# Kernel tuning notes

Measured on AMD Instinct MI355X. Metric: run time of the kernel, lower is better.

The kernel has to match this reference:

```python
import jax, jax.numpy as jnp
import numpy as np

N_NODES = 100000
N_EDGES = 1600000
IN_DIM = 256
HID = 128
ALPHA = 0.1
K_STEPS = 10


def setup_inputs() -> dict:
    key = jax.random.key(0)
    ks = jax.random.split(key, 10)
    x = jax.random.normal(ks[0], (N_NODES, IN_DIM), dtype=jnp.float32)
    edge_index = jax.random.randint(ks[1], (2, N_EDGES), 0, N_NODES, dtype=jnp.int64)
    s = 0.02
    W1 = jax.random.normal(ks[2], (HID, IN_DIM), dtype=jnp.float32) * s
    b1 = jnp.zeros((HID,), dtype=jnp.float32)
    W2 = jax.random.normal(ks[3], (HID, HID), dtype=jnp.float32) * s
    b2 = jnp.zeros((HID,), dtype=jnp.float32)
    W3 = jax.random.normal(ks[4], (HID, HID), dtype=jnp.float32) * s
    b3 = jnp.zeros((HID,), dtype=jnp.float32)
    Wo = jax.random.normal(ks[5], (1, HID), dtype=jnp.float32) * s
    bo = jnp.zeros((1,), dtype=jnp.float32)
    return {"x": x, "edge_index": edge_index, "W1": W1, "b1": b1,
            "W2": W2, "b2": b2, "W3": W3, "b3": b3, "Wo": Wo, "bo": bo}


def _gcn_norm(edge_index, num_nodes):
    # add self-loops, then symmetric normalization 1/sqrt(deg_i * deg_j)
    loop = jnp.arange(num_nodes, dtype=edge_index.dtype)
    src = jnp.concatenate([edge_index[0], loop])
    dst = jnp.concatenate([edge_index[1], loop])
    ones = jnp.ones(src.shape[0], dtype=jnp.float32)
    deg = jax.ops.segment_sum(ones, dst, num_segments=num_nodes)
    dinv = jnp.where(deg > 0, jax.lax.rsqrt(deg), 0.0)
    norm = dinv[src] * dinv[dst]
    return src, dst, norm


def reference(x, edge_index, W1, b1, W2, b2, W3, b3, Wo, bo):
    # MLP encoder (dropout=0 -> identity in eval)
    h = jax.nn.relu(x @ W1.T + b1)
    h = jax.nn.relu(h @ W2.T + b2)
    h = jax.nn.relu(h @ W3.T + b3)
    # APPNP propagation: h <- (1-alpha) * A_hat h + alpha * h0
    n = x.shape[0]
    src, dst, norm = _gcn_norm(edge_index, n)
    h0 = h
    for _ in range(K_STEPS):
        msg = norm[:, None] * h[src]            # [E+N, HID]
        agg = jax.ops.segment_sum(msg, dst, num_segments=n)
        h = (1.0 - ALPHA) * agg + ALPHA * h0
    out = h @ Wo.T + bo                          # [N, 1]
    return out.squeeze(-1)
```

## Files before the change

### kernel.cpp

```cpp
#include <hip/hip_runtime.h>

#define NN   100000
#define NE   1600000
#define IND  256
#define HIDD 128
#define BCAP 64
#define NPART 196
#define SCAP 10240
#define HPITCH 136

typedef __attribute__((ext_vector_type(8))) short short8v;
typedef __attribute__((ext_vector_type(4))) float f32x4;

__device__ inline unsigned packbf2(float x, float y) {
  unsigned xb = __float_as_uint(x);
  unsigned yb = __float_as_uint(y);
  xb += 0x7fffu + ((xb >> 16) & 1u);
  yb += 0x7fffu + ((yb >> 16) & 1u);
  return (xb >> 16) | (yb & 0xffff0000u);
}
__device__ inline unsigned short bf16r(float x) {
  unsigned b = __float_as_uint(x);
  b += 0x7fffu + ((b >> 16) & 1u);
  return (unsigned short)(b >> 16);
}

__global__ void wcvt_all(const float* __restrict__ W1, const float* __restrict__ W2,
                         const float* __restrict__ W3, unsigned* __restrict__ W1b,
                         unsigned* __restrict__ W2b, unsigned* __restrict__ W3b) {
  int i = blockIdx.x * 256 + threadIdx.x;
  const float* src; unsigned* dst; int off;
  if (i < 16384)      { src = W1; dst = W1b; off = i; }
  else if (i < 24576) { src = W2; dst = W2b; off = i - 16384; }
  else                { src = W3; dst = W3b; off = i - 24576; }
  float2 v = ((const float2*)src)[off];
  dst[off] = packbf2(v.x, v.y);
}

__global__ __launch_bounds__(256, 8) void fill_phaseA(
    const int* __restrict__ src, const int* __restrict__ dst,
    int* __restrict__ gcur, unsigned* __restrict__ sbuf)
{
  __shared__ int hist[NPART];
  __shared__ int lofs[NPART];
  const int tid = threadIdx.x;
  const int base = blockIdx.x * 2048;
  for (int i = tid; i < NPART; i += 256) hist[i] = 0;
  __syncthreads();
  int d[8], s[8];
#pragma unroll
  for (int i = 0; i < 8; ++i) {
    int e = base + i * 256 + tid;
    bool v = e < NE;
    d[i] = v ? dst[e] : -1;
    s[i] = v ? src[e] : 0;
    if (v) atomicAdd(&hist[d[i] >> 9], 1);
  }
  __syncthreads();
  for (int i = tid; i < NPART; i += 256)
    lofs[i] = atomicAdd(&gcur[i], hist[i]);
  __syncthreads();
#pragma unroll
  for (int i = 0; i < 8; ++i) {
    if (d[i] >= 0) {
      int p = d[i] >> 9;
      int q = atomicAdd(&lofs[p], 1);
      if (q < SCAP)
        sbuf[(size_t)p * SCAP + q] = ((unsigned)(d[i] & 511) << 17) | (unsigned)s[i];
    }
  }
}

__global__ __launch_bounds__(256, 8) void fill_phaseB(
    const unsigned* __restrict__ sbuf, const int* __restrict__ gcur,
    int* __restrict__ colbuk, int* __restrict__ deg)
{
  __shared__ int lcur[512];
  const int tid = threadIdx.x;
  const int b = blockIdx.x;
  for (int i = tid; i < 512; i += 256) lcur[i] = 0;
  __syncthreads();
  int cnt = min(gcur[b], SCAP);
  const unsigned* sp = sbuf + (size_t)b * SCAP;
  for (int i = tid; i < cnt; i += 256) {
    unsigned u = sp[i];
    int dloc = (int)(u >> 17);
    int s = (int)(u & 0x1FFFFu);
    int pos = atomicAdd(&lcur[dloc], 1);
    if (pos < BCAP) colbuk[(size_t)((b << 9) + dloc) * BCAP + pos] = s;
  }
  __syncthreads();
  for (int i = tid; i < 512; i += 256) {
    int node = (b << 9) + i;
    if (node < NN) deg[node] = lcur[i];
  }
}

__global__ __launch_bounds__(256) void enc_fused(
    const float* __restrict__ x,
    const unsigned short* __restrict__ W1b, const float* __restrict__ b1,
    const unsigned short* __restrict__ W2b, const float* __restrict__ b2,
    const unsigned short* __restrict__ W3b, const float* __restrict__ b3,
    const float* __restrict__ Wo, float* __restrict__ z)
{
  __shared__ unsigned short hbuf[128 * HPITCH];
  __shared__ float zsh[2][128];
  const int tid = threadIdx.x;
  const int lane = tid & 63, wid = tid >> 6;
  const int wr = wid >> 1, wc = wid & 1;
  const int bm = blockIdx.x * 128;
  const int lr = lane & 15, lg = lane >> 4;

  f32x4 acc[4][4];
#pragma unroll
  for (int i = 0; i < 4; ++i)
#pragma unroll
    for (int j = 0; j < 4; ++j) acc[i][j] = (f32x4){0.f, 0.f, 0.f, 0.f};

  for (int k0 = 0; k0 < IND; k0 += 32) {
    short8v a[4], b[4];
#pragma unroll
    for (int i = 0; i < 4; ++i) {
      int grow = bm + wr * 64 + i * 16 + lr;
      uint4 pk = make_uint4(0u, 0u, 0u, 0u);
      if (grow < NN) {
        const float* ap = x + (size_t)grow * IND + k0 + lg * 8;
        float4 v0 = ((const float4*)ap)[0];
        float4 v1 = ((const float4*)ap)[1];
        pk.x = packbf2(v0.x, v0.y); pk.y = packbf2(v0.z, v0.w);
        pk.z = packbf2(v1.x, v1.y); pk.w = packbf2(v1.z, v1.w);
      }
      a[i] = *(short8v*)&pk;
    }
#pragma unroll
    for (int j = 0; j < 4; ++j)
      b[j] = *(const short8v*)&W1b[(size_t)(wc * 64 + j * 16 + lr) * IND + k0 + lg * 8];
#pragma unroll
    for (int i = 0; i < 4; ++i)
#pragma unroll
      for (int j = 0; j < 4; ++j)
        acc[i][j] = __builtin_amdgcn_mfma_f32_16x16x32_bf16(a[i], b[j], acc[i][j], 0, 0, 0);
  }
#pragma unroll
  for (int i = 0; i < 4; ++i)
#pragma unroll
    for (int e = 0; e < 4; ++e) {
      int lrow = wr * 64 + i * 16 + lg * 4 + e;
#pragma unroll
      for (int j = 0; j < 4; ++j) {
        int cc = wc * 64 + j * 16 + lr;
        hbuf[lrow * HPITCH + cc] = bf16r(fmaxf(acc[i][j][e] + b1[cc], 0.f));
      }
    }
  __syncthreads();

#pragma unroll
  for (int i = 0; i < 4; ++i)
#pragma unroll
    for (int j = 0; j < 4; ++j) acc[i][j] = (f32x4){0.f, 0.f, 0.f, 0.f};
  for (int k0 = 0; k0 < HIDD; k0 += 32) {
    short8v a[4], b[4];
#pragma unroll
    for (int i = 0; i < 4; ++i)
      a[i] = *(const short8v*)&hbuf[(wr * 64 + i * 16 + lr) * HPITCH + k0 + lg * 8];
#pragma unroll
    for (int j = 0; j < 4; ++j)
      b[j] = *(const short8v*)&W2b[(size_t)(wc * 64 + j * 16 + lr) * HIDD + k0 + lg * 8];
#pragma unroll
    for (int i = 0; i < 4; ++i)
#pragma unroll
      for (int j = 0; j < 4; ++j)
        acc[i][j] = __builtin_amdgcn_mfma_f32_16x16x32_bf16(a[i], b[j], acc[i][j], 0, 0, 0);
  }
  __syncthreads();
#pragma unroll
  for (int i = 0; i < 4; ++i)
#pragma unroll
    for (int e = 0; e < 4; ++e) {
      int lrow = wr * 64 + i * 16 + lg * 4 + e;
#pragma unroll
      for (int j = 0; j < 4; ++j) {
        int cc = wc * 64 + j * 16 + lr;
        hbuf[lrow * HPITCH + cc] = bf16r(fmaxf(acc[i][j][e] + b2[cc], 0.f));
      }
    }
  __syncthreads();

#pragma unroll
  for (int i = 0; i < 4; ++i)
#pragma unroll
    for (int j = 0; j < 4; ++j) acc[i][j] = (f32x4){0.f, 0.f, 0.f, 0.f};
  for (int k0 = 0; k0 < HIDD; k0 += 32) {
    short8v a[4], b[4];
#pragma unroll
    for (int i = 0; i < 4; ++i)
      a[i] = *(const short8v*)&hbuf[(wr * 64 + i * 16 + lr) * HPITCH + k0 + lg * 8];
#pragma unroll
    for (int j = 0; j < 4; ++j)
      b[j] = *(const short8v*)&W3b[(size_t)(wc * 64 + j * 16 + lr) * HIDD + k0 + lg * 8];
#pragma unroll
    for (int i = 0; i < 4; ++i)
#pragma unroll
      for (int j = 0; j < 4; ++j)
        acc[i][j] = __builtin_amdgcn_mfma_f32_16x16x32_bf16(a[i], b[j], acc[i][j], 0, 0, 0);
  }
  float wv[4];
#pragma unroll
  for (int j = 0; j < 4; ++j) wv[j] = Wo[wc * 64 + j * 16 + lr];
  zsh[tid >> 7][tid & 127] = 0.f;
  __syncthreads();
#pragma unroll
  for (int i = 0; i < 4; ++i)
#pragma unroll
    for (int e = 0; e < 4; ++e) {
      float part = 0.f;
#pragma unroll
      for (int j = 0; j < 4; ++j) {
        int cc = wc * 64 + j * 16 + lr;
        part += fmaxf(acc[i][j][e] + b3[cc], 0.f) * wv[j];
      }
#pragma unroll
      for (int off = 8; off > 0; off >>= 1) part += __shfl_down(part, off, 16);
      if (lr == 0) zsh[wc][wr * 64 + i * 16 + lg * 4 + e] = part;
    }
  __syncthreads();
  if (tid < 128) {
    int row = bm + tid;
    if (row < NN) z[row] = zsh[0][tid] + zsh[1][tid];
  }
}

__global__ void prep_scalar(const int* __restrict__ deg, const float* __restrict__ z,
                            float* __restrict__ dinv, float* __restrict__ va) {
  int i = blockIdx.x * 256 + threadIdx.x;
  if (i < NN) {
    float di = rsqrtf((float)(deg[i] + 1));
    dinv[i] = di;
    va[i] = di * z[i];
  }
}

template<int LAST>
__global__ __launch_bounds__(256, 8) void appnp_sstep(
    const float* __restrict__ vin, const float* __restrict__ z,
    const float* __restrict__ dinv, const int* __restrict__ deg,
    const int* __restrict__ colbuk, float* __restrict__ vout,
    const float* __restrict__ bo, float* __restrict__ out)
{
  int tid = threadIdx.x;
  int sl = tid & 15;
  int node = blockIdx.x * 16 + (tid >> 4);
  if (node >= NN) return;
  int m = min(deg[node], BCAP);
  float val = (sl == 0) ? vin[node] : 0.f;
  for (int j = sl; j < m; j += 16)
    val += vin[colbuk[(size_t)node * BCAP + j]];
#pragma unroll
  for (int off = 8; off > 0; off >>= 1) val += __shfl_down(val, off, 16);
  if (sl == 0) {
    float di = dinv[node];
    float s = 0.9f * di * val + 0.1f * z[node];
    if (LAST) out[node] = s + bo[0];
    else vout[node] = di * s;
  }
}

extern "C" void kernel_launch(void* const* d_in, const int* in_sizes, int n_in,
                              void* d_out, int out_size, void* d_ws, size_t ws_size,
                              hipStream_t stream) {
  const float* x   = (const float*)d_in[0];
  const int*   ei  = (const int*)d_in[1];
  const float* W1  = (const float*)d_in[2];
  const float* b1  = (const float*)d_in[3];
  const float* W2  = (const float*)d_in[4];
  const float* b2  = (const float*)d_in[5];
  const float* W3  = (const float*)d_in[6];
  const float* b3  = (const float*)d_in[7];
  const float* Wo  = (const float*)d_in[8];
  const float* bo  = (const float*)d_in[9];
  float* out = (float*)d_out;

  const int* srcv = ei;
  const int* dstv = ei + NE;

  int*      colbuk = (int*)d_ws;
  unsigned* sbuf   = (unsigned*)(colbuk + (size_t)NN * BCAP);
  int*      gcur   = (int*)(sbuf + (size_t)NPART * SCAP);
  int*      deg    = gcur + NPART;
  float*    dinv   = (float*)(deg + NN);
  float*    zbuf   = dinv + NN;
  float*    va     = zbuf + NN;
  float*    vb     = va + NN;
  unsigned* W1b    = (unsigned*)(vb + NN);
  unsigned* W2b    = W1b + 16384;
  unsigned* W3b    = W2b + 8192;

  hipMemsetAsync(gcur, 0, NPART * 4, stream);

  wcvt_all<<<128, 256, 0, stream>>>(W1, W2, W3, W1b, W2b, W3b);

  fill_phaseA<<<(NE + 2047) / 2048, 256, 0, stream>>>(srcv, dstv, gcur, sbuf);
  fill_phaseB<<<NPART, 256, 0, stream>>>(sbuf, gcur, colbuk, deg);

  const int ng = (NN + 127) / 128;
  enc_fused<<<ng, 256, 0, stream>>>(x, (unsigned short*)W1b, b1,
                                    (unsigned short*)W2b, b2,
                                    (unsigned short*)W3b, b3, Wo, zbuf);

  prep_scalar<<<(NN + 255) / 256, 256, 0, stream>>>(deg, zbuf, dinv, va);

  int ssb = (NN + 15) / 16;
  float* cur = va; float* nxt = vb;
  for (int k = 0; k < 9; ++k) {
    appnp_sstep<0><<<ssb, 256, 0, stream>>>(cur, zbuf, dinv, deg, colbuk,
                                            nxt, nullptr, nullptr);
    float* t = cur; cur = nxt; nxt = t;
  }
  appnp_sstep<1><<<ssb, 256, 0, stream>>>(cur, zbuf, dinv, deg, colbuk,
                                          nullptr, bo, out);
}
```

Before: 235.9 us.

## Finer edge partitions, fuse degree/scalar prep, stage encoder input via LDS

Edge bucketing now uses 782 partitions of 128 nodes instead of 196 of 512, which gives fill_phaseB more blocks and smaller LDS counters. dinv is computed in fill_phaseB and the va scaling in enc_fused, so the prep_scalar kernel launch goes away. The first encoder GEMM stages the bf16-converted x tile through LDS with coalesced row loads instead of per-lane strided global reads. This adds two barriers per k-step, and SCAP=2500 per partition relies on there being few overflows given the random degree distribution.

```diff
diff --git a/kernel.cpp b/kernel.cpp
--- a/kernel.cpp
+++ b/kernel.cpp
@@ -5,8 +5,9 @@
 #define IND  256
 #define HIDD 128
 #define BCAP 64
-#define NPART 196
-#define SCAP 10240
+#define NPART 782
+#define SCAP 2500
+#define APITCH 40
 #define HPITCH 136
 
 typedef __attribute__((ext_vector_type(8))) short short8v;
@@ -54,31 +55,31 @@
     bool v = e < NE;
     d[i] = v ? dst[e] : -1;
     s[i] = v ? src[e] : 0;
-    if (v) atomicAdd(&hist[d[i] >> 9], 1);
+    if (v) atomicAdd(&hist[d[i] >> 7], 1);
   }
   __syncthreads();
   for (int i = tid; i < NPART; i += 256)
-    lofs[i] = atomicAdd(&gcur[i], hist[i]);
+    lofs[i] = hist[i] ? atomicAdd(&gcur[i], hist[i]) : 0;
   __syncthreads();
 #pragma unroll
   for (int i = 0; i < 8; ++i) {
     if (d[i] >= 0) {
-      int p = d[i] >> 9;
+      int p = d[i] >> 7;
       int q = atomicAdd(&lofs[p], 1);
       if (q < SCAP)
-        sbuf[(size_t)p * SCAP + q] = ((unsigned)(d[i] & 511) << 17) | (unsigned)s[i];
+        sbuf[(size_t)p * SCAP + q] = ((unsigned)(d[i] & 127) << 17) | (unsigned)s[i];
     }
   }
 }
 
 __global__ __launch_bounds__(256, 8) void fill_phaseB(
     const unsigned* __restrict__ sbuf, const int* __restrict__ gcur,
-    int* __restrict__ colbuk, int* __restrict__ deg)
+    int* __restrict__ colbuk, int* __restrict__ deg, float* __restrict__ dinv)
 {
-  __shared__ int lcur[512];
+  __shared__ int lcur[128];
   const int tid = threadIdx.x;
   const int b = blockIdx.x;
-  for (int i = tid; i < 512; i += 256) lcur[i] = 0;
+  if (tid < 128) lcur[tid] = 0;
   __syncthreads();
   int cnt = min(gcur[b], SCAP);
   const unsigned* sp = sbuf + (size_t)b * SCAP;
@@ -87,12 +88,16 @@
     int dloc = (int)(u >> 17);
     int s = (int)(u & 0x1FFFFu);
     int pos = atomicAdd(&lcur[dloc], 1);
-    if (pos < BCAP) colbuk[(size_t)((b << 9) + dloc) * BCAP + pos] = s;
-  }
-  __syncthreads();
-  for (int i = tid; i < 512; i += 256) {
-    int node = (b << 9) + i;
-    if (node < NN) deg[node] = lcur[i];
+    if (pos < BCAP) colbuk[(size_t)((b << 7) + dloc) * BCAP + pos] = s;
+  }
+  __syncthreads();
+  if (tid < 128) {
+    int node = (b << 7) + tid;
+    if (node < NN) {
+      int dg = lcur[tid];
+      deg[node] = dg;
+      dinv[node] = rsqrtf((float)(dg + 1));
+    }
   }
 }
 
@@ -101,10 +106,12 @@
     const unsigned short* __restrict__ W1b, const float* __restrict__ b1,
     const unsigned short* __restrict__ W2b, const float* __restrict__ b2,
     const unsigned short* __restrict__ W3b, const float* __restrict__ b3,
-    const float* __restrict__ Wo, float* __restrict__ z)
+    const float* __restrict__ Wo, const float* __restrict__ dinv,
+    float* __restrict__ z, float* __restrict__ va)
 {
   __shared__ unsigned short hbuf[128 * HPITCH];
   __shared__ float zsh[2][128];
+  unsigned short* lA = hbuf;
   const int tid = threadIdx.x;
   const int lane = tid & 63, wid = tid >> 6;
   const int wr = wid >> 1, wc = wid & 1;
@@ -118,28 +125,36 @@
     for (int j = 0; j < 4; ++j) acc[i][j] = (f32x4){0.f, 0.f, 0.f, 0.f};
 
   for (int k0 = 0; k0 < IND; k0 += 32) {
-    short8v a[4], b[4];
-#pragma unroll
-    for (int i = 0; i < 4; ++i) {
-      int grow = bm + wr * 64 + i * 16 + lr;
-      uint4 pk = make_uint4(0u, 0u, 0u, 0u);
+#pragma unroll
+    for (int s0 = 0; s0 < 512; s0 += 256) {
+      int s = s0 + tid, rr = s >> 2, g = s & 3;
+      int grow = bm + rr;
+      float4 v0 = make_float4(0.f, 0.f, 0.f, 0.f), v1 = v0;
       if (grow < NN) {
-        const float* ap = x + (size_t)grow * IND + k0 + lg * 8;
-        float4 v0 = ((const float4*)ap)[0];
-        float4 v1 = ((const float4*)ap)[1];
-        pk.x = packbf2(v0.x, v0.y); pk.y = packbf2(v0.z, v0.w);
-        pk.z = packbf2(v1.x, v1.y); pk.w = packbf2(v1.z, v1.w);
+        const float* ap = x + (size_t)grow * IND + k0 + g * 8;
+        v0 = ((const float4*)ap)[0]; v1 = ((const float4*)ap)[1];
       }
-      a[i] = *(short8v*)&pk;
-    }
-#pragma unroll
-    for (int j = 0; j < 4; ++j)
-      b[j] = *(const short8v*)&W1b[(size_t)(wc * 64 + j * 16 + lr) * IND + k0 + lg * 8];
-#pragma unroll
-    for (int i = 0; i < 4; ++i)
+      uint4 pk;
+      pk.x = packbf2(v0.x, v0.y); pk.y = packbf2(v0.z, v0.w);
+      pk.z = packbf2(v1.x, v1.y); pk.w = packbf2(v1.z, v1.w);
+      *(uint4*)&lA[rr * APITCH + g * 8] = pk;
+    }
+    __syncthreads();
+    {
+      short8v a[4], b[4];
+#pragma unroll
+      for (int i = 0; i < 4; ++i)
+        a[i] = *(const short8v*)&lA[(wr * 64 + i * 16 + lr) * APITCH + lg * 8];
 #pragma unroll
       for (int j = 0; j < 4; ++j)
-        acc[i][j] = __builtin_amdgcn_mfma_f32_16x16x32_bf16(a[i], b[j], acc[i][j], 0, 0, 0);
+        b[j] = *(const short8v*)&W1b[(size_t)(wc * 64 + j * 16 + lr) * IND + k0 + lg * 8];
+#pragma unroll
+      for (int i = 0; i < 4; ++i)
+#pragma unroll
+        for (int j = 0; j < 4; ++j)
+          acc[i][j] = __builtin_amdgcn_mfma_f32_16x16x32_bf16(a[i], b[j], acc[i][j], 0, 0, 0);
+    }
+    __syncthreads();
   }
 #pragma unroll
   for (int i = 0; i < 4; ++i)
@@ -226,17 +241,11 @@
   __syncthreads();
   if (tid < 128) {
     int row = bm + tid;
-    if (row < NN) z[row] = zsh[0][tid] + zsh[1][tid];
-  }
-}
-
-__global__ void prep_scalar(const int* __restrict__ deg, const float* __restrict__ z,
-                            float* __restrict__ dinv, float* __restrict__ va) {
-  int i = blockIdx.x * 256 + threadIdx.x;
-  if (i < NN) {
-    float di = rsqrtf((float)(deg[i] + 1));
-    dinv[i] = di;
-    va[i] = di * z[i];
+    if (row < NN) {
+      float zv = zsh[0][tid] + zsh[1][tid];
+      z[row] = zv;
+      va[row] = dinv[row] * zv;
+    }
   }
 }
 
@@ -300,14 +309,13 @@
   wcvt_all<<<128, 256, 0, stream>>>(W1, W2, W3, W1b, W2b, W3b);
 
   fill_phaseA<<<(NE + 2047) / 2048, 256, 0, stream>>>(srcv, dstv, gcur, sbuf);
-  fill_phaseB<<<NPART, 256, 0, stream>>>(sbuf, gcur, colbuk, deg);
+  fill_phaseB<<<NPART, 256, 0, stream>>>(sbuf, gcur, colbuk, deg, dinv);
 
   const int ng = (NN + 127) / 128;
   enc_fused<<<ng, 256, 0, stream>>>(x, (unsigned short*)W1b, b1,
                                     (unsigned short*)W2b, b2,
-                                    (unsigned short*)W3b, b3, Wo, zbuf);
-
-  prep_scalar<<<(NN + 255) / 256, 256, 0, stream>>>(deg, zbuf, dinv, va);
+                                    (unsigned short*)W3b, b3, Wo, dinv,
+                                    zbuf, va);
 
   int ssb = (NN + 15) / 16;
   float* cur = va; float* nxt = vb;
```

New measurement: 238.4 us. No clear change (+1.0%).

## Restructure encoder to per-wave 16-row tiles and fold scalar prep into fill

Applied to the files above, without the earlier changes.

The fused MLP encoder now gives each wave its own 16-row tile covering all 128 output columns, with private LDS scratch and no block-level barriers, instead of a 128-row block tile shared by four waves. The prep_scalar kernel is removed: its degree, dinv and initial-vector work moves into fill_phaseB, which now runs after the encoder so z is available. fill_phaseA also skips global atomics for empty histogram bins. The intent is to remove barrier stalls and one kernel launch. In exchange, each wave reloads the full weight matrices from global/L2 with less reuse per load, and the encoder row loop assumes NN is a multiple of 16.

```diff
diff --git a/kernel.cpp b/kernel.cpp
--- a/kernel.cpp
+++ b/kernel.cpp
@@ -7,7 +7,7 @@
 #define BCAP 64
 #define NPART 196
 #define SCAP 10240
-#define HPITCH 136
+#define HP   136
 
 typedef __attribute__((ext_vector_type(8))) short short8v;
 typedef __attribute__((ext_vector_type(4))) float f32x4;
@@ -58,7 +58,7 @@
   }
   __syncthreads();
   for (int i = tid; i < NPART; i += 256)
-    lofs[i] = atomicAdd(&gcur[i], hist[i]);
+    lofs[i] = hist[i] ? atomicAdd(&gcur[i], hist[i]) : 0;
   __syncthreads();
 #pragma unroll
   for (int i = 0; i < 8; ++i) {
@@ -73,7 +73,8 @@
 
 __global__ __launch_bounds__(256, 8) void fill_phaseB(
     const unsigned* __restrict__ sbuf, const int* __restrict__ gcur,
-    int* __restrict__ colbuk, int* __restrict__ deg)
+    const float* __restrict__ z, int* __restrict__ colbuk,
+    int* __restrict__ deg, float* __restrict__ dinv, float* __restrict__ va)
 {
   __shared__ int lcur[512];
   const int tid = threadIdx.x;
@@ -92,7 +93,13 @@
   __syncthreads();
   for (int i = tid; i < 512; i += 256) {
     int node = (b << 9) + i;
-    if (node < NN) deg[node] = lcur[i];
+    if (node < NN) {
+      int dg = lcur[i];
+      float di = rsqrtf((float)(dg + 1));
+      deg[node] = dg;
+      dinv[node] = di;
+      va[node] = di * z[node];
+    }
   }
 }
 
@@ -103,140 +110,91 @@
     const unsigned short* __restrict__ W3b, const float* __restrict__ b3,
     const float* __restrict__ Wo, float* __restrict__ z)
 {
-  __shared__ unsigned short hbuf[128 * HPITCH];
-  __shared__ float zsh[2][128];
+  __shared__ unsigned short hl[4][16 * HP];
   const int tid = threadIdx.x;
   const int lane = tid & 63, wid = tid >> 6;
-  const int wr = wid >> 1, wc = wid & 1;
-  const int bm = blockIdx.x * 128;
   const int lr = lane & 15, lg = lane >> 4;
-
-  f32x4 acc[4][4];
-#pragma unroll
-  for (int i = 0; i < 4; ++i)
-#pragma unroll
-    for (int j = 0; j < 4; ++j) acc[i][j] = (f32x4){0.f, 0.f, 0.f, 0.f};
-
-  for (int k0 = 0; k0 < IND; k0 += 32) {
-    short8v a[4], b[4];
-#pragma unroll
-    for (int i = 0; i < 4; ++i) {
-      int grow = bm + wr * 64 + i * 16 + lr;
-      uint4 pk = make_uint4(0u, 0u, 0u, 0u);
-      if (grow < NN) {
-        const float* ap = x + (size_t)grow * IND + k0 + lg * 8;
-        float4 v0 = ((const float4*)ap)[0];
-        float4 v1 = ((const float4*)ap)[1];
-        pk.x = packbf2(v0.x, v0.y); pk.y = packbf2(v0.z, v0.w);
-        pk.z = packbf2(v1.x, v1.y); pk.w = packbf2(v1.z, v1.w);
-      }
-      a[i] = *(short8v*)&pk;
-    }
-#pragma unroll
-    for (int j = 0; j < 4; ++j)
-      b[j] = *(const short8v*)&W1b[(size_t)(wc * 64 + j * 16 + lr) * IND + k0 + lg * 8];
-#pragma unroll
-    for (int i = 0; i < 4; ++i)
-#pragma unroll
-      for (int j = 0; j < 4; ++j)
-        acc[i][j] = __builtin_amdgcn_mfma_f32_16x16x32_bf16(a[i], b[j], acc[i][j], 0, 0, 0);
-  }
-#pragma unroll
-  for (int i = 0; i < 4; ++i)
-#pragma unroll
-    for (int e = 0; e < 4; ++e) {
-      int lrow = wr * 64 + i * 16 + lg * 4 + e;
-#pragma unroll
-      for (int j = 0; j < 4; ++j) {
-        int cc = wc * 64 + j * 16 + lr;
-        hbuf[lrow * HPITCH + cc] = bf16r(fmaxf(acc[i][j][e] + b1[cc], 0.f));
-      }
-    }
-  __syncthreads();
-
-#pragma unroll
-  for (int i = 0; i < 4; ++i)
-#pragma unroll
-    for (int j = 0; j < 4; ++j) acc[i][j] = (f32x4){0.f, 0.f, 0.f, 0.f};
-  for (int k0 = 0; k0 < HIDD; k0 += 32) {
-    short8v a[4], b[4];
-#pragma unroll
-    for (int i = 0; i < 4; ++i)
-      a[i] = *(const short8v*)&hbuf[(wr * 64 + i * 16 + lr) * HPITCH + k0 + lg * 8];
-#pragma unroll
-    for (int j = 0; j < 4; ++j)
-      b[j] = *(const short8v*)&W2b[(size_t)(wc * 64 + j * 16 + lr) * HIDD + k0 + lg * 8];
-#pragma unroll
-    for (int i = 0; i < 4; ++i)
-#pragma unroll
-      for (int j = 0; j < 4; ++j)
-        acc[i][j] = __builtin_amdgcn_mfma_f32_16x16x32_bf16(a[i], b[j], acc[i][j], 0, 0, 0);
-  }
-  __syncthreads();
-#pragma unroll
-  for (int i = 0; i < 4; ++i)
-#pragma unroll
-    for (int e = 0; e < 4; ++e) {
-      int lrow = wr * 64 + i * 16 + lg * 4 + e;
-#pragma unroll
-      for (int j = 0; j < 4; ++j) {
-        int cc = wc * 64 + j * 16 + lr;
-        hbuf[lrow * HPITCH + cc] = bf16r(fmaxf(acc[i][j][e] + b2[cc], 0.f));
-      }
-    }
-  __syncthreads();
-
-#pragma unroll
-  for (int i = 0; i < 4; ++i)
-#pragma unroll
-    for (int j = 0; j < 4; ++j) acc[i][j] = (f32x4){0.f, 0.f, 0.f, 0.f};
-  for (int k0 = 0; k0 < HIDD; k0 += 32) {
-    short8v a[4], b[4];
-#pragma unroll
-    for (int i = 0; i < 4; ++i)
-      a[i] = *(const short8v*)&hbuf[(wr * 64 + i * 16 + lr) * HPITCH + k0 + lg * 8];
-#pragma unroll
-    for (int j = 0; j < 4; ++j)
-      b[j] = *(const short8v*)&W3b[(size_t)(wc * 64 + j * 16 + lr) * HIDD + k0 + lg * 8];
-#pragma unroll
-    for (int i = 0; i < 4; ++i)
-#pragma unroll
-      for (int j = 0; j < 4; ++j)
-        acc[i][j] = __builtin_amdgcn_mfma_f32_16x16x32_bf16(a[i], b[j], acc[i][j], 0, 0, 0);
-  }
-  float wv[4];
-#pragma unroll
-  for (int j = 0; j < 4; ++j) wv[j] = Wo[wc * 64 + j * 16 + lr];
-  zsh[tid >> 7][tid & 127] = 0.f;
-  __syncthreads();
-#pragma unroll
-  for (int i = 0; i < 4; ++i)
-#pragma unroll
-    for (int e = 0; e < 4; ++e) {
-      float part = 0.f;
-#pragma unroll
-      for (int j = 0; j < 4; ++j) {
-        int cc = wc * 64 + j * 16 + lr;
-        part += fmaxf(acc[i][j][e] + b3[cc], 0.f) * wv[j];
-      }
-#pragma unroll
-      for (int off = 8; off > 0; off >>= 1) part += __shfl_down(part, off, 16);
-      if (lr == 0) zsh[wc][wr * 64 + i * 16 + lg * 4 + e] = part;
-    }
-  __syncthreads();
-  if (tid < 128) {
-    int row = bm + tid;
-    if (row < NN) z[row] = zsh[0][tid] + zsh[1][tid];
-  }
-}
-
-__global__ void prep_scalar(const int* __restrict__ deg, const float* __restrict__ z,
-                            float* __restrict__ dinv, float* __restrict__ va) {
-  int i = blockIdx.x * 256 + threadIdx.x;
-  if (i < NN) {
-    float di = rsqrtf((float)(deg[i] + 1));
-    dinv[i] = di;
-    va[i] = di * z[i];
+  const int rbase = (blockIdx.x * 4 + wid) * 16;
+  if (rbase >= NN) return;
+  unsigned short* hw = &hl[wid][0];
+
+  float b1v[8], b2v[8], b3v[8], wov[8];
+#pragma unroll
+  for (int j = 0; j < 8; ++j) {
+    int c = j * 16 + lr;
+    b1v[j] = b1[c]; b2v[j] = b2[c]; b3v[j] = b3[c]; wov[j] = Wo[c];
+  }
+
+  f32x4 acc[8];
+#pragma unroll
+  for (int j = 0; j < 8; ++j) acc[j] = (f32x4){0.f, 0.f, 0.f, 0.f};
+
+#pragma unroll
+  for (int k0 = 0; k0 < 8; ++k0) {
+    const float* ap = x + (size_t)(rbase + lr) * IND + k0 * 32 + lg * 8;
+    float4 v0 = ((const float4*)ap)[0];
+    float4 v1 = ((const float4*)ap)[1];
+    uint4 pk;
+    pk.x = packbf2(v0.x, v0.y); pk.y = packbf2(v0.z, v0.w);
+    pk.z = packbf2(v1.x, v1.y); pk.w = packbf2(v1.z, v1.w);
+    short8v a = *(short8v*)&pk;
+#pragma unroll
+    for (int j = 0; j < 8; ++j) {
+      short8v b = *(const short8v*)&W1b[(size_t)(j * 16 + lr) * IND + k0 * 32 + lg * 8];
+      acc[j] = __builtin_amdgcn_mfma_f32_16x16x32_bf16(a, b, acc[j], 0, 0, 0);
+    }
+  }
+#pragma unroll
+  for (int j = 0; j < 8; ++j)
+#pragma unroll
+    for (int e = 0; e < 4; ++e)
+      hw[(lg * 4 + e) * HP + j * 16 + lr] = bf16r(fmaxf(acc[j][e] + b1v[j], 0.f));
+
+#pragma unroll
+  for (int j = 0; j < 8; ++j) acc[j] = (f32x4){0.f, 0.f, 0.f, 0.f};
+#pragma unroll
+  for (int kk = 0; kk < 4; ++kk) {
+    short8v a = *(const short8v*)&hw[lr * HP + kk * 32 + lg * 8];
+#pragma unroll
+    for (int j = 0; j < 8; ++j) {
+      short8v b = *(const short8v*)&W2b[(size_t)(j * 16 + lr) * HIDD + kk * 32 + lg * 8];
+      acc[j] = __builtin_amdgcn_mfma_f32_16x16x32_bf16(a, b, acc[j], 0, 0, 0);
+    }
+  }
+#pragma unroll
+  for (int j = 0; j < 8; ++j)
+#pragma unroll
+    for (int e = 0; e < 4; ++e)
+      hw[(lg * 4 + e) * HP + j * 16 + lr] = bf16r(fmaxf(acc[j][e] + b2v[j], 0.f));
+
+#pragma unroll
+  for (int j = 0; j < 8; ++j) acc[j] = (f32x4){0.f, 0.f, 0.f, 0.f};
+#pragma unroll
+  for (int kk = 0; kk < 4; ++kk) {
+    short8v a = *(const short8v*)&hw[lr * HP + kk * 32 + lg * 8];
+#pragma unroll
+    for (int j = 0; j < 8; ++j) {
+      short8v b = *(const short8v*)&W3b[(size_t)(j * 16 + lr) * HIDD + kk * 32 + lg * 8];
+      acc[j] = __builtin_amdgcn_mfma_f32_16x16x32_bf16(a, b, acc[j], 0, 0, 0);
+    }
+  }
+  float part[4];
+#pragma unroll
+  for (int e = 0; e < 4; ++e) {
+    float p = 0.f;
+#pragma unroll
+    for (int j = 0; j < 8; ++j)
+      p += fmaxf(acc[j][e] + b3v[j], 0.f) * wov[j];
+    part[e] = p;
+  }
+#pragma unroll
+  for (int off = 8; off > 0; off >>= 1)
+#pragma unroll
+    for (int e = 0; e < 4; ++e)
+      part[e] += __shfl_down(part[e], off, 16);
+  if (lr == 0) {
+    float4 v = make_float4(part[0], part[1], part[2], part[3]);
+    *(float4*)&z[rbase + lg * 4] = v;
   }
 }
 
@@ -300,14 +258,13 @@
   wcvt_all<<<128, 256, 0, stream>>>(W1, W2, W3, W1b, W2b, W3b);
 
   fill_phaseA<<<(NE + 2047) / 2048, 256, 0, stream>>>(srcv, dstv, gcur, sbuf);
-  fill_phaseB<<<NPART, 256, 0, stream>>>(sbuf, gcur, colbuk, deg);
-
-  const int ng = (NN + 127) / 128;
+
+  const int ng = (NN / 16 + 3) / 4;
   enc_fused<<<ng, 256, 0, stream>>>(x, (unsigned short*)W1b, b1,
                                     (unsigned short*)W2b, b2,
                                     (unsigned short*)W3b, b3, Wo, zbuf);
 
-  prep_scalar<<<(NN + 255) / 256, 256, 0, stream>>>(deg, zbuf, dinv, va);
+  fill_phaseB<<<NPART, 256, 0, stream>>>(sbuf, gcur, zbuf, colbuk, deg, dinv, va);
 
   int ssb = (NN + 15) / 16;
   float* cur = va; float* nxt = vb;
```

Result: slower. 275.9 us (+17.0%).
